# Optimization experiments

Measured on AMD Instinct MI355X. Metric: run time of the kernel, lower is better.

## Reference

```python
import jax, jax.numpy as jnp
import numpy as np

D_MODEL = 1024
NUM_HEADS = 16
HEAD_DIM = D_MODEL // NUM_HEADS


def setup_inputs() -> dict:
    key = jax.random.key(0)
    ks = jax.random.split(key, 6)
    B, S = 2, 2048
    s = 1.0 / np.sqrt(D_MODEL)
    return {
        "x": jax.random.normal(ks[0], (B, S, D_MODEL), dtype=jnp.float32),
        "Wq": jax.random.normal(ks[1], (D_MODEL, D_MODEL), dtype=jnp.float32) * s,
        "Wk": jax.random.normal(ks[2], (D_MODEL, D_MODEL), dtype=jnp.float32) * s,
        "Wv": jax.random.normal(ks[3], (D_MODEL, D_MODEL), dtype=jnp.float32) * s,
        "Wo": jax.random.normal(ks[4], (D_MODEL, D_MODEL), dtype=jnp.float32) * s,
        "bo": jax.random.normal(ks[5], (D_MODEL,), dtype=jnp.float32) * 0.01,
    }


def reference(x, Wq, Wk, Wv, Wo, bo):
    b, n, _ = x.shape
    # QKV projections (no bias, qkv_bias=False); weights applied as x @ W^T like nn.Linear
    q = (x @ Wq.T).reshape(b, n, NUM_HEADS, HEAD_DIM).transpose(0, 2, 1, 3)  # [b,h,n,d]
    k = (x @ Wk.T).reshape(b, n, NUM_HEADS, HEAD_DIM).transpose(0, 2, 1, 3)
    v = (x @ Wv.T).reshape(b, n, NUM_HEADS, HEAD_DIM).transpose(0, 2, 1, 3)
    scores = jnp.einsum("bhqd,bhkd->bhqk", q, k)
    causal = jnp.tril(jnp.ones((n, n), dtype=bool))  # keep where True
    scores = jnp.where(causal, scores, -jnp.inf)
    weights = jax.nn.softmax(scores / np.sqrt(HEAD_DIM), axis=-1)
    # dropout p=0.0 -> identity (eval semantics)
    ctx = jnp.einsum("bhqk,bhkd->bhqd", weights, v)
    ctx = ctx.transpose(0, 2, 1, 3).reshape(b, n, D_MODEL)
    return ctx @ Wo.T + bo
```

## Files before the change

### kernel.cpp

```cpp
#include <hip/hip_runtime.h>

#define D_MODEL 1024
#define NUM_HEADS 16
#define HEAD_DIM 64
#define BATCH 2
#define SEQ 2048
#define MTOT (BATCH * SEQ)

typedef __attribute__((ext_vector_type(8))) short bf16x8;
typedef __attribute__((ext_vector_type(4))) short s16x4;
typedef __attribute__((ext_vector_type(4))) float f32x4;
typedef unsigned short u16;
typedef unsigned long long u64;

__device__ __forceinline__ u16 f2bf(float f) {
    unsigned u = __float_as_uint(f);
    return (u16)((u + 0x7FFFu + ((u >> 16) & 1u)) >> 16);
}

__device__ __forceinline__ unsigned cvt_pk_bf16(float lo, float hi) {
    unsigned r;
    asm volatile("v_cvt_pk_bf16_f32 %0, %1, %2" : "=v"(r) : "v"(lo), "v"(hi));
    return r;
}

#if __has_builtin(__builtin_amdgcn_exp2f)
#define EXP2(x) __builtin_amdgcn_exp2f(x)
#else
#define EXP2(x) exp2f(x)
#endif

#define GLOAD16(gp, lp) __builtin_amdgcn_global_load_lds(                      \
    (const __attribute__((address_space(1))) void*)(gp),                       \
    (__attribute__((address_space(3))) void*)(lp), 16, 0, 0)

__global__ __launch_bounds__(256)
void cast_all_kernel(const float* __restrict__ x,  const float* __restrict__ Wq,
                     const float* __restrict__ Wk, const float* __restrict__ Wv,
                     const float* __restrict__ Wo, u16* __restrict__ dst)
{
    const int i = blockIdx.x * 256 + threadIdx.x;
    const float* src;
    int j;
    if (i < 524288) { src = x; j = i; }
    else if (i < 917504) {
        const int k = i - 524288;
        const int z = k >> 17;
        src = (z == 0) ? Wq : (z == 1) ? Wk : Wv;
        j = k & 0x1FFFF;
    } else { src = Wo; j = i - 917504; }
    const float4* s = reinterpret_cast<const float4*>(src) + (size_t)j * 2;
    float4 a = s[0], b = s[1];
    u16 tmp[8] = {f2bf(a.x), f2bf(a.y), f2bf(a.z), f2bf(a.w),
                  f2bf(b.x), f2bf(b.y), f2bf(b.z), f2bf(b.w)};
    *reinterpret_cast<int4*>(dst + (size_t)i * 8) = *reinterpret_cast<int4*>(tmp);
}

__global__ __launch_bounds__(256)
void gemm_qkv_kernel(const u16* __restrict__ A, const u16* __restrict__ B,
                     u16* __restrict__ Qo, u16* __restrict__ Ko, u16* __restrict__ Vt)
{
    __shared__ u16 Al[128 * 64];
    __shared__ u16 Bl[128 * 64];

    const int tid = threadIdx.x;
    const int l = tid & 63;
    const int w = tid >> 6;
    const int wm = w >> 1, wn = w & 1;
    const int lr = l & 15, lg = l >> 4;
    const int m0 = blockIdx.y * 128;
    const int n0 = blockIdx.x * 128;

    const int srow = tid >> 3;
    const int scol = ((tid & 7) ^ (srow & 7)) * 8;
    const int sxa = (lr & 7) * 8;

    f32x4 acc[4][4];
    #pragma unroll
    for (int i = 0; i < 4; ++i)
        #pragma unroll
        for (int j = 0; j < 4; ++j) acc[i][j] = (f32x4){0.f, 0.f, 0.f, 0.f};

    for (int k0 = 0; k0 < D_MODEL; k0 += 64) {
        __syncthreads();
        #pragma unroll
        for (int i = 0; i < 4; ++i) {
            const u16* ga = A + (size_t)(m0 + i * 32 + srow) * D_MODEL + k0 + scol;
            const u16* gb = B + (size_t)(n0 + i * 32 + srow) * D_MODEL + k0 + scol;
            GLOAD16(ga, Al + i * 2048 + w * 512);
            GLOAD16(gb, Bl + i * 2048 + w * 512);
        }
        __syncthreads();
        #pragma unroll
        for (int kc = 0; kc < 2; ++kc) {
            bf16x8 af[4], bfr[4];
            #pragma unroll
            for (int i = 0; i < 4; ++i)
                af[i] = *reinterpret_cast<const bf16x8*>(
                    &Al[(wm * 64 + i * 16 + lr) * 64 + ((kc * 32 + lg * 8) ^ sxa)]);
            #pragma unroll
            for (int j = 0; j < 4; ++j)
                bfr[j] = *reinterpret_cast<const bf16x8*>(
                    &Bl[(wn * 64 + j * 16 + lr) * 64 + ((kc * 32 + lg * 8) ^ sxa)]);
            #pragma unroll
            for (int i = 0; i < 4; ++i)
                #pragma unroll
                for (int j = 0; j < 4; ++j)
                    acc[i][j] = __builtin_amdgcn_mfma_f32_16x16x32_bf16(
                        af[i], bfr[j], acc[i][j], 0, 0, 0);
        }
    }

    const int z = (n0 >> 10);
    if (z < 2) {
        #pragma unroll
        for (int i = 0; i < 4; ++i) {
            #pragma unroll
            for (int r = 0; r < 4; ++r) {
                const int m = m0 + wm * 64 + i * 16 + lg * 4 + r;
                const int bb = m >> 11, s = m & (SEQ - 1);
                #pragma unroll
                for (int j = 0; j < 4; ++j) {
                    const int c = n0 + wn * 64 + j * 16 + lr;
                    const int cc = c & 1023, h = cc >> 6, d = cc & 63;
                    const size_t idx = ((size_t)(bb * NUM_HEADS + h) * SEQ + s) * 64 + d;
                    if (z == 0) Qo[idx] = f2bf(acc[i][j][r] * 0.18033688f);
                    else        Ko[idx] = f2bf(acc[i][j][r]);
                }
            }
        }
    } else {
        #pragma unroll
        for (int i = 0; i < 4; ++i) {
            const int mbase = m0 + wm * 64 + i * 16 + lg * 4;
            const int bb = mbase >> 11, s = mbase & (SEQ - 1);
            #pragma unroll
            for (int j = 0; j < 4; ++j) {
                const int c = n0 + wn * 64 + j * 16 + lr;
                const int cc = c & 1023, h = cc >> 6, d = cc & 63;
                u16 t4[4];
                #pragma unroll
                for (int r = 0; r < 4; ++r) t4[r] = f2bf(acc[i][j][r]);
                *reinterpret_cast<u64*>(
                    &Vt[((size_t)(bb * NUM_HEADS + h) * 64 + d) * SEQ + s]) =
                    *reinterpret_cast<u64*>(t4);
            }
        }
    }
}

__global__ __launch_bounds__(256)
void gemm_out_kernel(const u16* __restrict__ A, const u16* __restrict__ B,
                     const float* __restrict__ bias, float* __restrict__ out)
{
    __shared__ u16 Al[128 * 64];
    __shared__ u16 Bl[128 * 64];

    const int tid = threadIdx.x;
    const int l = tid & 63;
    const int w = tid >> 6;
    const int wm = w >> 1, wn = w & 1;
    const int lr = l & 15, lg = l >> 4;
    const int m0 = blockIdx.y * 128;
    const int n0 = blockIdx.x * 128;

    const int srow = tid >> 3;
    const int scol = ((tid & 7) ^ (srow & 7)) * 8;
    const int sxa = (lr & 7) * 8;

    f32x4 acc[4][4];
    #pragma unroll
    for (int i = 0; i < 4; ++i)
        #pragma unroll
        for (int j = 0; j < 4; ++j) acc[i][j] = (f32x4){0.f, 0.f, 0.f, 0.f};

    for (int k0 = 0; k0 < D_MODEL; k0 += 64) {
        __syncthreads();
        #pragma unroll
        for (int i = 0; i < 4; ++i) {
            const u16* ga = A + (size_t)(m0 + i * 32 + srow) * D_MODEL + k0 + scol;
            const u16* gb = B + (size_t)(n0 + i * 32 + srow) * D_MODEL + k0 + scol;
            GLOAD16(ga, Al + i * 2048 + w * 512);
            GLOAD16(gb, Bl + i * 2048 + w * 512);
        }
        __syncthreads();
        #pragma unroll
        for (int kc = 0; kc < 2; ++kc) {
            bf16x8 af[4], bfr[4];
            #pragma unroll
            for (int i = 0; i < 4; ++i)
                af[i] = *reinterpret_cast<const bf16x8*>(
                    &Al[(wm * 64 + i * 16 + lr) * 64 + ((kc * 32 + lg * 8) ^ sxa)]);
            #pragma unroll
            for (int j = 0; j < 4; ++j)
                bfr[j] = *reinterpret_cast<const bf16x8*>(
                    &Bl[(wn * 64 + j * 16 + lr) * 64 + ((kc * 32 + lg * 8) ^ sxa)]);
            #pragma unroll
            for (int i = 0; i < 4; ++i)
                #pragma unroll
                for (int j = 0; j < 4; ++j)
                    acc[i][j] = __builtin_amdgcn_mfma_f32_16x16x32_bf16(
                        af[i], bfr[j], acc[i][j], 0, 0, 0);
        }
    }

    #pragma unroll
    for (int i = 0; i < 4; ++i) {
        #pragma unroll
        for (int r = 0; r < 4; ++r) {
            const int m = m0 + wm * 64 + i * 16 + lg * 4 + r;
            #pragma unroll
            for (int j = 0; j < 4; ++j) {
                const int c = n0 + wn * 64 + j * 16 + lr;
                out[(size_t)m * D_MODEL + c] = acc[i][j][r] + bias[c];
            }
        }
    }
}

__global__ __launch_bounds__(256)
void attn_kernel(const u16* __restrict__ Q, const u16* __restrict__ K,
                 const u16* __restrict__ Vt, u16* __restrict__ ctx)
{
    __shared__ char LdsB[2][16384];

    const int tid = threadIdx.x;
    const int l = tid & 63;
    const int w = tid >> 6;
    const int lr = l & 15;
    const int lg = l >> 4;

    const int xcd  = blockIdx.x & 7;
    const int slot = blockIdx.x >> 3;
    const int bh   = xcd * 4 + (slot >> 5);
    const int qtb  = 31 - (slot & 31);
    const size_t hbase = (size_t)bh * SEQ * 64;
    const int b = bh >> 4, h = bh & (NUM_HEADS - 1);
    const u16* __restrict__ Kh = K + hbase;
    const u16* __restrict__ Vh = Vt + hbase;

    const int q0 = qtb * 64;
    const int qrow = q0 + w * 16 + lr;

    const int r0 = tid >> 3;
    const int c0 = ((tid & 7) ^ (r0 & 7)) * 8;
    const int r1 = (256 + tid) >> 3;
    const int c1 = ((tid & 7) ^ (r1 & 7)) * 8;
    const int d0b = tid * 16;
    const int d1b = 4096 + tid * 16;
    const int rswz = (lr & 7) << 4;

    bf16x8 qf0, qf1;
    {
        const u16* qp = Q + hbase + (size_t)qrow * 64 + lg * 8;
        qf0 = *reinterpret_cast<const bf16x8*>(qp);
        qf1 = *reinterpret_cast<const bf16x8*>(qp + 32);
    }

    f32x4 oacc[4];
    #pragma unroll
    for (int nb = 0; nb < 4; ++nb) oacc[nb] = (f32x4){0.f, 0.f, 0.f, 0.f};
    float lsum = 0.f;

    {
        char* kb = LdsB[0];
        char* vb = LdsB[0] + 8192;
        GLOAD16(Kh + (size_t)r0 * 64 + c0, kb + d0b);
        GLOAD16(Kh + (size_t)r1 * 64 + c1, kb + d1b);
        GLOAD16(Vh + (size_t)r0 * SEQ + c0, vb + d0b);
        GLOAD16(Vh + (size_t)r1 * SEQ + c1, vb + d1b);
    }

    for (int it = 0; it <= qtb; ++it) {
        const int buf = it & 1;
        if (it < qtb) {
            const int kb64 = (it + 1) * 64;
            char* kbl = LdsB[buf ^ 1];
            char* vbl = kbl + 8192;
            GLOAD16(Kh + (size_t)(kb64 + r0) * 64 + c0, kbl + d0b);
            GLOAD16(Kh + (size_t)(kb64 + r1) * 64 + c1, kbl + d1b);
            GLOAD16(Vh + (size_t)r0 * SEQ + kb64 + c0, vbl + d0b);
            GLOAD16(Vh + (size_t)r1 * SEQ + kb64 + c1, vbl + d1b);
            asm volatile("s_waitcnt vmcnt(4)" ::: "memory");
        } else {
            asm volatile("s_waitcnt vmcnt(0)" ::: "memory");
        }
        __builtin_amdgcn_s_barrier();

        const char* kbuf = LdsB[buf];
        const char* vbuf = kbuf + 8192;

        f32x4 s[4];
        __builtin_amdgcn_s_setprio(1);
        #pragma unroll
        for (int m = 0; m < 4; ++m) {
            s[m] = (f32x4){0.f, 0.f, 0.f, 0.f};
            const char* krow = kbuf + (16 * m + lr) * 128;
            bf16x8 kf0 = *reinterpret_cast<const bf16x8*>(krow + ((lg * 16) ^ rswz));
            bf16x8 kf1 = *reinterpret_cast<const bf16x8*>(krow + ((64 + lg * 16) ^ rswz));
            s[m] = __builtin_amdgcn_mfma_f32_16x16x32_bf16(kf0, qf0, s[m], 0, 0, 0);
            s[m] = __builtin_amdgcn_mfma_f32_16x16x32_bf16(kf1, qf1, s[m], 0, 0, 0);
        }
        __builtin_amdgcn_s_setprio(0);

        if (it == qtb) {
            #pragma unroll
            for (int m = 0; m < 4; ++m)
                #pragma unroll
                for (int r = 0; r < 4; ++r)
                    if (16 * m + 4 * lg + r > 16 * w + lr) s[m][r] = -1.0e38f;
        }

        float p[4][4];
        #pragma unroll
        for (int m = 0; m < 4; ++m)
            #pragma unroll
            for (int r = 0; r < 4; ++r) p[m][r] = EXP2(s[m][r]);

        {
            float a0 = (p[0][0] + p[0][1]) + (p[0][2] + p[0][3]);
            float a1 = (p[1][0] + p[1][1]) + (p[1][2] + p[1][3]);
            float a2 = (p[2][0] + p[2][1]) + (p[2][2] + p[2][3]);
            float a3 = (p[3][0] + p[3][1]) + (p[3][2] + p[3][3]);
            lsum += (a0 + a1) + (a2 + a3);
        }

        unsigned dw[4][2];
        #pragma unroll
        for (int m = 0; m < 4; ++m) {
            dw[m][0] = cvt_pk_bf16(p[m][0], p[m][1]);
            dw[m][1] = cvt_pk_bf16(p[m][2], p[m][3]);
        }

        __builtin_amdgcn_s_setprio(1);
        #pragma unroll
        for (int c = 0; c < 2; ++c) {
            union { unsigned u[4]; bf16x8 v; } pb;
            pb.u[0] = dw[2 * c][0];     pb.u[1] = dw[2 * c][1];
            pb.u[2] = dw[2 * c + 1][0]; pb.u[3] = dw[2 * c + 1][1];
            #pragma unroll
            for (int nb = 0; nb < 4; ++nb) {
                const char* vrow = vbuf + (16 * nb + lr) * 128;
                union { s16x4 hv[2]; bf16x8 v; } vf;
                vf.hv[0] = *reinterpret_cast<const s16x4*>(
                    vrow + ((c * 64 + lg * 8) ^ rswz));
                vf.hv[1] = *reinterpret_cast<const s16x4*>(
                    vrow + ((c * 64 + 32 + lg * 8) ^ rswz));
                oacc[nb] = __builtin_amdgcn_mfma_f32_16x16x32_bf16(
                    vf.v, pb.v, oacc[nb], 0, 0, 0);
            }
        }
        __builtin_amdgcn_s_setprio(0);

        __builtin_amdgcn_s_barrier();
    }

    lsum += __shfl_xor(lsum, 16);
    lsum += __shfl_xor(lsum, 32);
    const float inv = 1.0f / lsum;

    u16* op = ctx + ((size_t)(b * SEQ) + qrow) * D_MODEL + h * 64 + 4 * lg;
    #pragma unroll
    for (int nb = 0; nb < 4; ++nb) {
        u16 t4[4];
        #pragma unroll
        for (int r = 0; r < 4; ++r) t4[r] = f2bf(oacc[nb][r] * inv);
        *reinterpret_cast<u64*>(op + 16 * nb) = *reinterpret_cast<u64*>(t4);
    }
}


extern "C" void kernel_launch(void* const* d_in, const int* in_sizes, int n_in,
                              void* d_out, int out_size, void* d_ws, size_t ws_size,
                              hipStream_t stream)
{
    const float* x  = (const float*)d_in[0];
    const float* Wq = (const float*)d_in[1];
    const float* Wk = (const float*)d_in[2];
    const float* Wv = (const float*)d_in[3];
    const float* Wo = (const float*)d_in[4];
    const float* bo = (const float*)d_in[5];
    float* out = (float*)d_out;

    u16* xb   = (u16*)d_ws;
    u16* wqkv = xb   + (size_t)MTOT * D_MODEL;
    u16* wob  = wqkv + (size_t)3 * D_MODEL * D_MODEL;
    u16* Qw   = wob  + (size_t)D_MODEL * D_MODEL;
    u16* Kw   = Qw   + (size_t)MTOT * D_MODEL;
    u16* Vtw  = Kw   + (size_t)MTOT * D_MODEL;
    u16* ctxb = Vtw  + (size_t)MTOT * D_MODEL;

    cast_all_kernel<<<4096, 256, 0, stream>>>(x, Wq, Wk, Wv, Wo, xb);

    dim3 gq(3 * D_MODEL / 128, MTOT / 128);
    gemm_qkv_kernel<<<gq, 256, 0, stream>>>(xb, wqkv, Qw, Kw, Vtw);

    attn_kernel<<<dim3(1024), 256, 0, stream>>>(Qw, Kw, Vtw, ctxb);

    dim3 go(D_MODEL / 128, MTOT / 128);
    gemm_out_kernel<<<go, 256, 0, stream>>>(ctxb, wob, bo, out);
}
```

Measured before the change: 129.5 us.

## Split causal attention KV range into chunks with separate reduction kernel

Long query tiles now have their KV range split into up to four chunks processed by separate blocks (split-K / flash-decoding style), so the launch goes from 1024 to 2560 blocks with more even work per block. Partial unnormalized outputs (bf16) and row sums are written to workspace, and a new reduce kernel sums them and normalizes. This targets load imbalance and tail effects from the triangular causal workload. In exchange it adds an extra launch, workspace traffic, and bf16 rounding of partial outputs. The softmax uses no running max, so partials can be summed directly.

```diff
diff --git a/kernel.cpp b/kernel.cpp
--- a/kernel.cpp
+++ b/kernel.cpp
@@ -16,6 +16,9 @@
 __device__ __forceinline__ u16 f2bf(float f) {
     unsigned u = __float_as_uint(f);
     return (u16)((u + 0x7FFFu + ((u >> 16) & 1u)) >> 16);
+}
+__device__ __forceinline__ float bf2f(u16 v) {
+    return __uint_as_float((unsigned)v << 16);
 }
 
 __device__ __forceinline__ unsigned cvt_pk_bf16(float lo, float hi) {
@@ -218,9 +221,17 @@
     }
 }
 
+__device__ __forceinline__ void map_pair(int p, int& qt, int& ch) {
+    if (p < 32)      { qt = 31 - (p >> 2); ch = p & 3; }
+    else if (p < 56) { int t = p - 32; qt = 23 - t / 3; ch = t % 3; }
+    else if (p < 72) { int t = p - 56; qt = 15 - (t >> 1); ch = t & 1; }
+    else             { qt = 79 - p; ch = 0; }
+}
+
 __global__ __launch_bounds__(256)
 void attn_kernel(const u16* __restrict__ Q, const u16* __restrict__ K,
-                 const u16* __restrict__ Vt, u16* __restrict__ ctx)
+                 const u16* __restrict__ Vt, u16* __restrict__ ctx,
+                 u16* __restrict__ Opart, float* __restrict__ Lpart)
 {
     __shared__ char LdsB[2][16384];
 
@@ -232,14 +243,22 @@
 
     const int xcd  = blockIdx.x & 7;
     const int slot = blockIdx.x >> 3;
-    const int bh   = xcd * 4 + (slot >> 5);
-    const int qtb  = 31 - (slot & 31);
+    const int bh   = xcd * 4 + slot / 80;
+    int qt, ch;
+    map_pair(slot % 80, qt, ch);
+
+    const int ntiles = qt + 1;
+    const int nch  = (qt + 8) >> 3;
+    const int base = ntiles / nch, rem = ntiles % nch;
+    const int start = ch * base + (ch < rem ? ch : rem);
+    const int cnt   = base + (ch < rem ? 1 : 0);
+
     const size_t hbase = (size_t)bh * SEQ * 64;
     const int b = bh >> 4, h = bh & (NUM_HEADS - 1);
     const u16* __restrict__ Kh = K + hbase;
     const u16* __restrict__ Vh = Vt + hbase;
 
-    const int q0 = qtb * 64;
+    const int q0 = qt * 64;
     const int qrow = q0 + w * 16 + lr;
 
     const int r0 = tid >> 3;
@@ -265,16 +284,18 @@
     {
         char* kb = LdsB[0];
         char* vb = LdsB[0] + 8192;
-        GLOAD16(Kh + (size_t)r0 * 64 + c0, kb + d0b);
-        GLOAD16(Kh + (size_t)r1 * 64 + c1, kb + d1b);
-        GLOAD16(Vh + (size_t)r0 * SEQ + c0, vb + d0b);
-        GLOAD16(Vh + (size_t)r1 * SEQ + c1, vb + d1b);
-    }
-
-    for (int it = 0; it <= qtb; ++it) {
+        const int kb64 = start * 64;
+        GLOAD16(Kh + (size_t)(kb64 + r0) * 64 + c0, kb + d0b);
+        GLOAD16(Kh + (size_t)(kb64 + r1) * 64 + c1, kb + d1b);
+        GLOAD16(Vh + (size_t)r0 * SEQ + kb64 + c0, vb + d0b);
+        GLOAD16(Vh + (size_t)r1 * SEQ + kb64 + c1, vb + d1b);
+    }
+
+    for (int it = 0; it < cnt; ++it) {
+        const int tile = start + it;
         const int buf = it & 1;
-        if (it < qtb) {
-            const int kb64 = (it + 1) * 64;
+        if (it < cnt - 1) {
+            const int kb64 = (tile + 1) * 64;
             char* kbl = LdsB[buf ^ 1];
             char* vbl = kbl + 8192;
             GLOAD16(Kh + (size_t)(kb64 + r0) * 64 + c0, kbl + d0b);
@@ -303,7 +324,7 @@
         }
         __builtin_amdgcn_s_setprio(0);
 
-        if (it == qtb) {
+        if (tile == qt) {
             #pragma unroll
             for (int m = 0; m < 4; ++m)
                 #pragma unroll
@@ -357,15 +378,66 @@
 
     lsum += __shfl_xor(lsum, 16);
     lsum += __shfl_xor(lsum, 32);
-    const float inv = 1.0f / lsum;
-
-    u16* op = ctx + ((size_t)(b * SEQ) + qrow) * D_MODEL + h * 64 + 4 * lg;
+
+    if (nch == 1) {
+        const float inv = 1.0f / lsum;
+        u16* op = ctx + ((size_t)(b * SEQ) + qrow) * D_MODEL + h * 64 + 4 * lg;
+        #pragma unroll
+        for (int nb = 0; nb < 4; ++nb) {
+            u16 t4[4];
+            #pragma unroll
+            for (int r = 0; r < 4; ++r) t4[r] = f2bf(oacc[nb][r] * inv);
+            *reinterpret_cast<u64*>(op + 16 * nb) = *reinterpret_cast<u64*>(t4);
+        }
+    } else {
+        const int slot4 = ((bh * 24 + (qt - 8)) << 2) + ch;
+        u16* op = Opart + (size_t)slot4 * 4096 + (w * 16 + lr) * 64 + 4 * lg;
+        #pragma unroll
+        for (int nb = 0; nb < 4; ++nb) {
+            u16 t4[4];
+            #pragma unroll
+            for (int r = 0; r < 4; ++r) t4[r] = f2bf(oacc[nb][r]);
+            *reinterpret_cast<u64*>(op + 16 * nb) = *reinterpret_cast<u64*>(t4);
+        }
+        if (lg == 0) Lpart[slot4 * 64 + w * 16 + lr] = lsum;
+    }
+}
+
+__global__ __launch_bounds__(64)
+void attn_reduce_kernel(const u16* __restrict__ Opart,
+                        const float* __restrict__ Lpart,
+                        u16* __restrict__ ctx)
+{
+    const int blk = blockIdx.x;
+    const int bh = blk / 24, qt8 = blk % 24;
+    const int qt = qt8 + 8;
+    const int nch = (qt + 8) >> 3;
+    const int t = threadIdx.x;
+    const int b = bh >> 4, h = bh & (NUM_HEADS - 1);
+    const int slot0 = (bh * 24 + qt8) << 2;
+
+    float acc[64] = {};
+    float lt = 0.f;
+    for (int ch = 0; ch < nch; ++ch) {
+        const u16* op = Opart + (size_t)(slot0 + ch) * 4096 + t * 64;
+        lt += Lpart[(slot0 + ch) * 64 + t];
+        #pragma unroll
+        for (int cchunk = 0; cchunk < 8; ++cchunk) {
+            u16 v[8];
+            *reinterpret_cast<int4*>(v) =
+                *reinterpret_cast<const int4*>(op + cchunk * 8);
+            #pragma unroll
+            for (int j = 0; j < 8; ++j) acc[cchunk * 8 + j] += bf2f(v[j]);
+        }
+    }
+    const float inv = 1.0f / lt;
+    u16* orow = ctx + ((size_t)(b * SEQ) + qt * 64 + t) * D_MODEL + h * 64;
     #pragma unroll
-    for (int nb = 0; nb < 4; ++nb) {
-        u16 t4[4];
-        #pragma unroll
-        for (int r = 0; r < 4; ++r) t4[r] = f2bf(oacc[nb][r] * inv);
-        *reinterpret_cast<u64*>(op + 16 * nb) = *reinterpret_cast<u64*>(t4);
+    for (int cchunk = 0; cchunk < 8; ++cchunk) {
+        u16 v[8];
+        #pragma unroll
+        for (int j = 0; j < 8; ++j) v[j] = f2bf(acc[cchunk * 8 + j] * inv);
+        *reinterpret_cast<int4*>(orow + cchunk * 8) = *reinterpret_cast<int4*>(v);
     }
 }
 
@@ -389,13 +461,16 @@
     u16* Kw   = Qw   + (size_t)MTOT * D_MODEL;
     u16* Vtw  = Kw   + (size_t)MTOT * D_MODEL;
     u16* ctxb = Vtw  + (size_t)MTOT * D_MODEL;
+    u16* Opart = ctxb + (size_t)MTOT * D_MODEL;
+    float* Lpart = (float*)(Opart + (size_t)3072 * 4096);
 
     cast_all_kernel<<<4096, 256, 0, stream>>>(x, Wq, Wk, Wv, Wo, xb);
 
     dim3 gq(3 * D_MODEL / 128, MTOT / 128);
     gemm_qkv_kernel<<<gq, 256, 0, stream>>>(xb, wqkv, Qw, Kw, Vtw);
 
-    attn_kernel<<<dim3(1024), 256, 0, stream>>>(Qw, Kw, Vtw, ctxb);
+    attn_kernel<<<dim3(2560), 256, 0, stream>>>(Qw, Kw, Vtw, ctxb, Opart, Lpart);
+    attn_reduce_kernel<<<dim3(768), 64, 0, stream>>>(Opart, Lpart, ctxb);
 
     dim3 go(D_MODEL / 128, MTOT / 128);
     gemm_out_kernel<<<go, 256, 0, stream>>>(ctxb, wob, bo, out);
```

New measurement: 121.6 us. 1.06x faster.
